# Optimization experiments

Hardware: AMD Instinct MI355X
Metric: run time of the kernel (lower is better)

The kernel has to match this reference:

```python
import jax, jax.numpy as jnp
import numpy as np

SOFTCAP = 50.0
EPS = 1e-6
N_HEADS, D_HEAD = 16, 64


def _rms(x, w):
    return x * jax.lax.rsqrt(jnp.mean(x * x, axis=-1, keepdims=True) + EPS) * w


def _rope(x, cos, sin):
    # Faithful to source: apply_rope uses x.size(1) as the position axis, but is
    # called on (B, H, T, Dh) tensors, so positions are indexed by HEAD index.
    n = x.shape[1]
    x1, x2 = x[..., 0::2], x[..., 1::2]
    c = cos[:n][None, :, None, :]
    s = sin[:n][None, :, None, :]
    return jnp.stack([x1 * c - x2 * s, x1 * s + x2 * c], axis=-1).reshape(x.shape)


def setup_inputs() -> dict:
    key = jax.random.key(0)
    ks = jax.random.split(key, 12)
    L, D, H, Dh, Dff, V, B, T = 6, 1024, N_HEADS, D_HEAD, 4096, 32000, 1, 1024
    r = lambda k, shape: jax.random.normal(k, shape, dtype=jnp.float32) * 0.02
    return {
        'x': jax.random.randint(ks[0], (B, T), 0, V, dtype=jnp.int32),
        'embed': r(ks[1], (V, D)),
        'ln1': jnp.ones((L, D), jnp.float32),
        'Wq': r(ks[2], (L, H * Dh, D)),
        'Wk': r(ks[3], (L, H * Dh, D)),
        'Wv': r(ks[4], (L, H * Dh, D)),
        'Wo': r(ks[5], (L, D, H * Dh)),
        'qn': jnp.ones((L, Dh), jnp.float32),
        'kn': jnp.ones((L, Dh), jnp.float32),
        'ln2': jnp.ones((L, D), jnp.float32),
        'Wg': r(ks[6], (L, Dff, D)),
        'Wu': r(ks[7], (L, Dff, D)),
        'Wd': r(ks[8], (L, D, Dff)),
        'ln_out': jnp.ones((D,), jnp.float32),
    }


def reference(x, embed, ln1, Wq, Wk, Wv, Wo, qn, kn, ln2, Wg, Wu, Wd, ln_out):
    B, T = x.shape
    H, Dh = N_HEADS, D_HEAD
    scale = Dh ** -0.5
    # RoPE tables (theta=10000)
    freqs = 1.0 / (10000.0 ** (jnp.arange(0, Dh, 2, dtype=jnp.float32) / Dh))
    ang = jnp.arange(T, dtype=jnp.float32)[:, None] * freqs[None, :]
    cos, sin = jnp.cos(ang), jnp.sin(ang)
    mask = jnp.triu(jnp.ones((T, T), dtype=bool), k=1)  # True above diagonal

    h = embed[x]  # (B, T, D)

    def block(h, p):
        l1, wq, wk, wv, wo, qnw, knw, l2, wg, wu, wd = p
        hn = _rms(h, l1)
        q = (hn @ wq.T).reshape(B, T, H, Dh).transpose(0, 2, 1, 3)  # (B,H,T,Dh)
        k = (hn @ wk.T).reshape(B, T, H, Dh).transpose(0, 2, 1, 3)
        v = (hn @ wv.T).reshape(B, T, H, Dh).transpose(0, 2, 1, 3)
        q = _rope(_rms(q, qnw), cos, sin)
        k = _rope(_rms(k, knw), cos, sin)
        scores = jnp.einsum('bhtd,bhsd->bhts', q, k) * scale
        scores = SOFTCAP * jnp.tanh(scores / SOFTCAP)
        scores = jnp.where(mask[None, None], -jnp.inf, scores)
        attn = jax.nn.softmax(scores, axis=-1)
        o = jnp.einsum('bhts,bhsd->bhtd', attn, v)
        o = o.transpose(0, 2, 1, 3).reshape(B, T, H * Dh)
        h = h + o @ wo.T
        hn2 = _rms(h, l2)
        h = h + (jax.nn.silu(hn2 @ wg.T) * (hn2 @ wu.T)) @ wd.T
        return h, None

    h, _ = jax.lax.scan(block, h, (ln1, Wq, Wk, Wv, Wo, qn, kn, ln2, Wg, Wu, Wd))
    # tied embed/head
    logits = _rms(h, ln_out) @ embed.T  # (B, T, V)
    return logits
```

## Files before the change

### kernel.cpp

```cpp
#include <hip/hip_runtime.h>
#include <math.h>
#include <type_traits>

typedef __bf16 bf16_t;
typedef bf16_t bf16x4 __attribute__((ext_vector_type(4)));
typedef bf16_t bf16x8 __attribute__((ext_vector_type(8)));
typedef float  f32x4  __attribute__((ext_vector_type(4)));

#define RMS_EPS 1e-6f

enum { EP_STORE = 0, EP_RESID = 1, EP_SPLIT = 2, EP_SILU = 3 };

template<int V> using IC = std::integral_constant<int, V>;

static __device__ __forceinline__ f32x4 mfma16(bf16x8 a, bf16x8 b, f32x4 c) {
    return __builtin_amdgcn_mfma_f32_16x16x32_bf16(a, b, c, 0, 0, 0);
}

#define GLDS(gp, lp) __builtin_amdgcn_global_load_lds( \
    (const __attribute__((address_space(1))) void*)(gp), \
    (__attribute__((address_space(3))) void*)(lp), 16, 0, 0)

template<int N> static __device__ __forceinline__ void vmwait() {
    if constexpr (N == 0)      asm volatile("s_waitcnt vmcnt(0)" ::: "memory");
    else if constexpr (N == 2) asm volatile("s_waitcnt vmcnt(2)" ::: "memory");
    else if constexpr (N == 3) asm volatile("s_waitcnt vmcnt(3)" ::: "memory");
    else if constexpr (N == 4) asm volatile("s_waitcnt vmcnt(4)" ::: "memory");
    else if constexpr (N == 6) asm volatile("s_waitcnt vmcnt(6)" ::: "memory");
    else if constexpr (N == 8) asm volatile("s_waitcnt vmcnt(8)" ::: "memory");
    __builtin_amdgcn_sched_barrier(0);
}
static __device__ __forceinline__ void bar() { __builtin_amdgcn_s_barrier(); }

template<int BM, int BN, int WR, int WC, int PLANES, int EPIL>
__global__ __launch_bounds__(WR * WC * 64,
    (WR * WC == 8) ? 4 : ((PLANES >= 2 && BM == 128) ? 3 : 4))
void gemm_bf16(const bf16_t* __restrict__ Ah, const bf16_t* __restrict__ Al,
               const bf16_t* __restrict__ Bh,
               float* __restrict__ Cf, bf16_t* __restrict__ Ch, bf16_t* __restrict__ Cl,
               int K, int lda, int ldb, int ldc, long long sC)
{
    constexpr int ASZ = BM * 32, BSZ = BN * 32;
    constexpr int NW = WR * WC;
    constexpr int NLD = (BM / 16 * (PLANES >= 2 ? 2 : 1) + BN / 16) / NW;
    __shared__ __align__(16) bf16_t sAh[2][ASZ], sBh[2][BSZ];
    __shared__ __align__(16) bf16_t sAl[PLANES >= 2 ? 2 : 1][PLANES >= 2 ? ASZ : 8];

    const int gx = gridDim.x;
    int id = blockIdx.x + gx * blockIdx.y;
    if (gridDim.z == 1) {
        int nwg = gx * gridDim.y;
        int q = nwg >> 3, r = nwg & 7;
        int xcd = id & 7, ix = id >> 3;
        id = (xcd < r ? xcd * (q + 1) : r * (q + 1) + (xcd - r) * q) + ix;
    }
    const int bm = id % gx, bn = id / gx;
    const int row0 = bm * BM, col0 = bn * BN;

    const size_t kofs = (size_t)blockIdx.z * K;
    Ah += kofs;  Bh += kofs;
    if constexpr (PLANES >= 2) Al += kofs;

    const int tid = threadIdx.x, lane = tid & 63, wave = tid >> 6;
    const int lr = lane & 15, lg = lane >> 4;
    constexpr int WM = BM / WR, WN = BN / WC, MF = WM / 16, NF = WN / 16;
    const int wr = wave / WC, wc = wave % WC;

    f32x4 acc[MF][NF];
    #pragma unroll
    for (int m = 0; m < MF; ++m)
        #pragma unroll
        for (int n = 0; n < NF; ++n) acc[m][n] = (f32x4){0.f, 0.f, 0.f, 0.f};

    auto stage = [&](int k0, auto pc) {
        constexpr int p = decltype(pc)::value;
        #pragma unroll
        for (int i = wave; i < BM / 16; i += NW) {
            int s = i * 64 + lane, rr = s >> 2, c = s & 3;
            size_t go = (size_t)(row0 + rr) * lda + k0 + ((c ^ ((rr >> 1) & 3)) << 3);
            GLDS(Ah + go, &sAh[p][i * 512]);
            if constexpr (PLANES >= 2) GLDS(Al + go, &sAl[p][i * 512]);
        }
        #pragma unroll
        for (int i = wave; i < BN / 16; i += NW) {
            int s = i * 64 + lane, rr = s >> 2, c = s & 3;
            size_t go = (size_t)(col0 + rr) * ldb + k0 + ((c ^ ((rr >> 1) & 3)) << 3);
            GLDS(Bh + go, &sBh[p][i * 512]);
        }
    };

    auto compute = [&](auto pc) {
        constexpr int p = decltype(pc)::value;
        bf16x8 ahf[MF], alf[MF], bhf[NF];
        #pragma unroll
        for (int m = 0; m < MF; ++m) {
            int rr = wr * WM + m * 16 + lr;
            int by = rr * 64 + ((lg ^ ((rr >> 1) & 3)) << 4);
            ahf[m] = *(const bf16x8*)((const char*)&sAh[p][0] + by);
            if constexpr (PLANES >= 2)
                alf[m] = *(const bf16x8*)((const char*)&sAl[p][0] + by);
        }
        #pragma unroll
        for (int n = 0; n < NF; ++n) {
            int rr = wc * WN + n * 16 + lr;
            int by = rr * 64 + ((lg ^ ((rr >> 1) & 3)) << 4);
            bhf[n] = *(const bf16x8*)((const char*)&sBh[p][0] + by);
        }
        #pragma unroll
        for (int m = 0; m < MF; ++m)
            #pragma unroll
            for (int n = 0; n < NF; ++n) {
                acc[m][n] = mfma16(ahf[m], bhf[n], acc[m][n]);
                if constexpr (PLANES >= 2)
                    acc[m][n] = mfma16(alf[m], bhf[n], acc[m][n]);
            }
    };

    stage(0, IC<0>{});
    int k0 = 32;
    for (; k0 + 32 < K; k0 += 64) {
        stage(k0, IC<1>{});
        vmwait<NLD>(); bar();
        compute(IC<0>{});
        bar();
        stage(k0 + 32, IC<0>{});
        vmwait<NLD>(); bar();
        compute(IC<1>{});
        bar();
    }
    stage(k0, IC<1>{});
    vmwait<NLD>(); bar();
    compute(IC<0>{});
    bar();
    vmwait<0>(); bar();
    compute(IC<1>{});

    #pragma unroll
    for (int m = 0; m < MF; ++m)
        #pragma unroll
        for (int n = 0; n < NF; ++n)
            #pragma unroll
            for (int r = 0; r < 4; ++r) {
                int grow = row0 + wr * WM + m * 16 + lg * 4 + r;
                int gcol = col0 + wc * WN + n * 16 + lr;
                float v = acc[m][n][r];
                if constexpr (EPIL == EP_SILU) {
                    float pv = __shfl_xor(v, 1, 64);
                    if (!(lr & 1)) {
                        float s = (v / (1.0f + expf(-v))) * pv;
                        size_t off = (size_t)grow * ldc + (gcol >> 1);
                        Ch[off] = (bf16_t)s;
                    }
                } else {
                    size_t off = (size_t)blockIdx.z * sC + (size_t)grow * ldc + gcol;
                    if constexpr (EPIL == EP_STORE) {
                        Cf[off] = v;
                    } else if constexpr (EPIL == EP_RESID) {
                        Cf[off] += v;
                    } else {
                        bf16_t hb = (bf16_t)v;
                        Ch[off] = hb;
                        Cl[off] = (bf16_t)(v - (float)hb);
                    }
                }
            }
}

__global__ __launch_bounds__(512, 4)
void gemm_logits(const bf16_t* __restrict__ Ah, const bf16_t* __restrict__ Bh,
                 float* __restrict__ Cf)
{
    constexpr int lda = 1024, ldb = 1024, ldc = 32000;
    __shared__ __align__(16) bf16_t sA[3][128 * 32], sB[3][256 * 32];

    const int gx = gridDim.x;
    int id = blockIdx.x + gx * blockIdx.y;
    {
        int nwg = gx * gridDim.y;
        int q = nwg >> 3, r = nwg & 7;
        int xcd = id & 7, ix = id >> 3;
        id = (xcd < r ? xcd * (q + 1) : r * (q + 1) + (xcd - r) * q) + ix;
    }
    const int bm = id % gx, bn = id / gx;
    const int row0 = bm * 128, col0 = bn * 256;

    const int tid = threadIdx.x, lane = tid & 63, wave = tid >> 6;
    const int lr = lane & 15, lg = lane >> 4;
    const int wr = wave >> 2, wc = wave & 3;

    f32x4 acc[4][4];
    #pragma unroll
    for (int m = 0; m < 4; ++m)
        #pragma unroll
        for (int n = 0; n < 4; ++n) acc[m][n] = (f32x4){0.f, 0.f, 0.f, 0.f};

    auto stage = [&](int k0, int p) {
        {
            int i = wave;
            int s = i * 64 + lane, rr = s >> 2, c = s & 3;
            size_t go = (size_t)(row0 + rr) * lda + k0 + ((c ^ ((rr >> 1) & 3)) << 3);
            GLDS(Ah + go, &sA[p][i * 512]);
        }
        #pragma unroll
        for (int i = wave; i < 16; i += 8) {
            int s = i * 64 + lane, rr = s >> 2, c = s & 3;
            size_t go = (size_t)(col0 + rr) * ldb + k0 + ((c ^ ((rr >> 1) & 3)) << 3);
            GLDS(Bh + go, &sB[p][i * 512]);
        }
    };

    auto compute = [&](int p) {
        bf16x8 af[4], bf[4];
        #pragma unroll
        for (int m = 0; m < 4; ++m) {
            int rr = wr * 64 + m * 16 + lr;
            int by = rr * 64 + ((lg ^ ((rr >> 1) & 3)) << 4);
            af[m] = *(const bf16x8*)((const char*)&sA[p][0] + by);
        }
        #pragma unroll
        for (int n = 0; n < 4; ++n) {
            int rr = wc * 64 + n * 16 + lr;
            int by = rr * 64 + ((lg ^ ((rr >> 1) & 3)) << 4);
            bf[n] = *(const bf16x8*)((const char*)&sB[p][0] + by);
        }
        #pragma unroll
        for (int m = 0; m < 4; ++m)
            #pragma unroll
            for (int n = 0; n < 4; ++n)
                acc[m][n] = mfma16(af[m], bf[n], acc[m][n]);
    };

    stage(0, 0);
    stage(32, 1);
    for (int j = 0; j < 30; ++j) {
        stage(32 * (j + 2), (j + 2) % 3);
        vmwait<6>(); bar();
        compute(j % 3);
        bar();
    }
    vmwait<3>(); bar();
    compute(0);
    vmwait<0>(); bar();
    compute(1);

    #pragma unroll
    for (int m = 0; m < 4; ++m)
        #pragma unroll
        for (int n = 0; n < 4; ++n)
            #pragma unroll
            for (int r = 0; r < 4; ++r) {
                int grow = row0 + wr * 64 + m * 16 + lg * 4 + r;
                int gcol = col0 + wc * 64 + n * 16 + lr;
                Cf[(size_t)grow * ldc + gcol] = acc[m][n][r];
            }
}

static __device__ __forceinline__ void wsplit_body(
    int b2, int tid,
    const float* wq, const float* wk, const float* wv, const float* wo,
    const float* wg, const float* wu, const float* wd,
    bf16_t* wAh, bf16_t* wGUh, bf16_t* wdh)
{
    #pragma unroll
    for (int k = 0; k < 4; ++k) {
        int b = b2 * 4 + k;
        const float* src;
        bf16_t* dst;
        size_t so, doff;
        if (b < 4096) {
            src = b < 1024 ? wq : b < 2048 ? wk : b < 3072 ? wv : wo;
            so = (size_t)(b & 1023) * 256 + tid;
            doff = (size_t)b * 256 + tid;
            dst = wAh;
        } else if (b < 12288) {
            int bb = b - 4096;
            int row = bb < 4096 ? 2 * bb : 2 * (bb - 4096) + 1;
            src = bb < 4096 ? wg : wu;
            so = (size_t)(bb & 4095) * 256 + tid;
            doff = (size_t)row * 256 + tid;
            dst = wGUh;
        } else {
            src = wd;
            so = (size_t)(b - 12288) * 256 + tid;
            doff = so;
            dst = wdh;
        }
        f32x4 v = ((const f32x4*)src)[so];
        bf16x4 hv;
        #pragma unroll
        for (int j = 0; j < 4; ++j) hv[j] = (bf16_t)v[j];
        ((bf16x4*)dst)[doff] = hv;
    }
}

__global__ __launch_bounds__(256)
void reduce_rms_wsplit(const float* __restrict__ p, float* __restrict__ h,
                       const float* __restrict__ w, bf16_t* __restrict__ outh,
                       const float* wq, const float* wk, const float* wv,
                       const float* wo, const float* wg, const float* wu,
                       const float* wd, bf16_t* wAh, bf16_t* wGUh, bf16_t* wdh)
{
    int blk = blockIdx.x, tid = threadIdx.x;
    if (blk >= 1024) {
        if (wq) wsplit_body(blk - 1024, tid, wq, wk, wv, wo, wg, wu, wd,
                            wAh, wGUh, wdh);
        return;
    }
    size_t i = (size_t)blk * 256 + tid;
    const size_t S = (1024 * 1024) / 4;
    f32x4 a = ((const f32x4*)p)[i];
    f32x4 b = ((const f32x4*)p)[i + S];
    f32x4 c = ((const f32x4*)p)[i + 2 * S];
    f32x4 d = ((const f32x4*)p)[i + 3 * S];
    f32x4 hv = ((const f32x4*)h)[i];
    #pragma unroll
    for (int j = 0; j < 4; ++j) hv[j] += (a[j] + b[j]) + (c[j] + d[j]);
    ((f32x4*)h)[i] = hv;

    float ss = hv[0]*hv[0] + hv[1]*hv[1] + hv[2]*hv[2] + hv[3]*hv[3];
    #pragma unroll
    for (int m = 1; m < 64; m <<= 1) ss += __shfl_xor(ss, m, 64);
    __shared__ float red[4];
    if ((tid & 63) == 0) red[tid >> 6] = ss;
    __syncthreads();
    float tot = red[0] + red[1] + red[2] + red[3];
    float inv = rsqrtf(tot * (1.0f / 1024.0f) + RMS_EPS);
    f32x4 wt4 = *(const f32x4*)(w + tid * 4);
    bf16x4 hv4;
    #pragma unroll
    for (int j = 0; j < 4; ++j) hv4[j] = (bf16_t)(hv[j] * inv * wt4[j]);
    ((bf16x4*)outh)[i] = hv4;
}

__global__ __launch_bounds__(256)
void gather_rms_wsplit(const int* __restrict__ ids, const float* __restrict__ embed,
                       const float* __restrict__ w, float* __restrict__ h,
                       bf16_t* __restrict__ outh,
                       const float* wq, const float* wk, const float* wv,
                       const float* wo, const float* wg, const float* wu,
                       const float* wd, bf16_t* wAh, bf16_t* wGUh, bf16_t* wdh)
{
    int blk = blockIdx.x, tid = threadIdx.x;
    if (blk >= 1024) {
        wsplit_body(blk - 1024, tid, wq, wk, wv, wo, wg, wu, wd, wAh, wGUh, wdh);
        return;
    }
    int row = ids[blk];
    f32x4 v = ((const f32x4*)(embed + (size_t)row * 1024))[tid];
    ((f32x4*)(h + (size_t)blk * 1024))[tid] = v;

    float ss = v[0]*v[0] + v[1]*v[1] + v[2]*v[2] + v[3]*v[3];
    #pragma unroll
    for (int m = 1; m < 64; m <<= 1) ss += __shfl_xor(ss, m, 64);
    __shared__ float red[4];
    if ((tid & 63) == 0) red[tid >> 6] = ss;
    __syncthreads();
    float tot = red[0] + red[1] + red[2] + red[3];
    float inv = rsqrtf(tot * (1.0f / 1024.0f) + RMS_EPS);
    f32x4 wt4 = *(const f32x4*)(w + tid * 4);
    bf16x4 hv;
    #pragma unroll
    for (int j = 0; j < 4; ++j) hv[j] = (bf16_t)(v[j] * inv * wt4[j]);
    ((bf16x4*)outh)[(size_t)blk * 256 + tid] = hv;
}

__global__ __launch_bounds__(128, 2)
void flash_attn(const bf16_t* __restrict__ qkvh,
                const bf16_t* __restrict__ vTh, const bf16_t* __restrict__ vTl,
                bf16_t* __restrict__ oh)
{
    __shared__ __align__(16) bf16_t sQ[32*64], sK[64*64], sVh[64*64], sVl[64*64];
    __shared__ __align__(16) bf16_t sPh[32*64], sPl[32*64];

    const int q0 = blockIdx.x * 32;
    const int hh = blockIdx.y;
    const int tid = threadIdx.x, lane = tid & 63, w = tid >> 6;
    const int lr = lane & 15, lg = lane >> 4;

    #pragma unroll
    for (int ii = 0; ii < 2; ++ii) {
        int r0 = w * 16 + ii * 8;
        int r  = r0 + (lane >> 3);
        int i  = lane & 7;
        GLDS(qkvh + (size_t)(q0 + r) * 3072 + hh * 64 + ((i ^ (r & 7)) << 3),
             sQ + r0 * 64);
    }
    __syncthreads();

    bf16x8 qa[2];
    #pragma unroll
    for (int ks = 0; ks < 2; ++ks) {
        int r = w * 16 + lr;
        qa[ks] = *(const bf16x8*)((const char*)sQ + r * 128 +
                                  ((((ks << 2) | lg) ^ (r & 7)) << 4));
    }

    f32x4 o_acc[4];
    #pragma unroll
    for (int n = 0; n < 4; ++n) o_acc[n] = (f32x4){0.f, 0.f, 0.f, 0.f};
    float m_run[4] = {-1e30f, -1e30f, -1e30f, -1e30f};
    float l_run[4] = {0.f, 0.f, 0.f, 0.f};

    const int ntiles = ((q0 + 31) >> 6) + 1;
    for (int t = 0; t < ntiles; ++t) {
        const int kv0 = t * 64;
        #pragma unroll
        for (int ii = 0; ii < 4; ++ii) {
            int r0 = w * 32 + ii * 8;
            int r  = r0 + (lane >> 3);
            int i  = lane & 7;
            GLDS(qkvh + (size_t)(kv0 + r) * 3072 + 1024 + hh * 64 + ((i ^ (r & 7)) << 3),
                 sK + r0 * 64);
            GLDS(vTh + (size_t)(hh * 64 + r) * 1024 + kv0 + ((i ^ (r & 7)) << 3),
                 sVh + r0 * 64);
            GLDS(vTl + (size_t)(hh * 64 + r) * 1024 + kv0 + ((i ^ (r & 7)) << 3),
                 sVl + r0 * 64);
        }
        __syncthreads();

        f32x4 s_acc[4];
        #pragma unroll
        for (int n = 0; n < 4; ++n) s_acc[n] = (f32x4){0.f, 0.f, 0.f, 0.f};
        #pragma unroll
        for (int ks = 0; ks < 2; ++ks)
            #pragma unroll
            for (int n = 0; n < 4; ++n) {
                int r = n * 16 + lr;
                bf16x8 kb = *(const bf16x8*)((const char*)sK + r * 128 +
                                             ((((ks << 2) | lg) ^ (r & 7)) << 4));
                s_acc[n] = mfma16(qa[ks], kb, s_acc[n]);
            }

        #pragma unroll
        for (int j = 0; j < 4; ++j) {
            int qr = q0 + w * 16 + lg * 4 + j;
            float p[4];
            float mx = -1e30f;
            #pragma unroll
            for (int n = 0; n < 4; ++n) {
                float v = s_acc[n][j] * 0.125f;
                v = 50.f * tanhf(v * 0.02f);
                int key = kv0 + n * 16 + lr;
                if (key > qr) v = -1e30f;
                p[n] = v;
                mx = fmaxf(mx, v);
            }
            #pragma unroll
            for (int m = 1; m < 16; m <<= 1) mx = fmaxf(mx, __shfl_xor(mx, m, 64));
            float mn = fmaxf(m_run[j], mx);
            float ef = __expf(m_run[j] - mn);
            m_run[j] = mn;
            float rs = 0.f;
            #pragma unroll
            for (int n = 0; n < 4; ++n) {
                float e = expf(p[n] - mn);
                p[n] = e;
                rs += e;
            }
            #pragma unroll
            for (int m = 1; m < 16; m <<= 1) rs += __shfl_xor(rs, m, 64);
            l_run[j] = l_run[j] * ef + rs;
            #pragma unroll
            for (int n = 0; n < 4; ++n) o_acc[n][j] *= ef;
            int r = w * 16 + lg * 4 + j;
            #pragma unroll
            for (int n = 0; n < 4; ++n) {
                int c = n * 16 + lr;
                int byo = r * 128 + ((((c >> 3) ^ (r & 7)) << 4)) + ((c & 7) << 1);
                bf16_t hb = (bf16_t)p[n];
                *(bf16_t*)((char*)sPh + byo) = hb;
                *(bf16_t*)((char*)sPl + byo) = (bf16_t)(p[n] - (float)hb);
            }
        }

        #pragma unroll
        for (int ks = 0; ks < 2; ++ks) {
            int pr = w * 16 + lr;
            int pby = pr * 128 + ((((ks << 2) | lg) ^ (pr & 7)) << 4);
            bf16x8 pa  = *(const bf16x8*)((const char*)sPh + pby);
            bf16x8 pl_ = *(const bf16x8*)((const char*)sPl + pby);
            #pragma unroll
            for (int n = 0; n < 4; ++n) {
                int vr = n * 16 + lr;
                int vby = vr * 128 + ((((ks << 2) | lg) ^ (vr & 7)) << 4);
                bf16x8 vhf = *(const bf16x8*)((const char*)sVh + vby);
                bf16x8 vlf = *(const bf16x8*)((const char*)sVl + vby);
                o_acc[n] = mfma16(pa,  vhf, o_acc[n]);
                o_acc[n] = mfma16(pl_, vhf, o_acc[n]);
                o_acc[n] = mfma16(pa,  vlf, o_acc[n]);
            }
        }
        __syncthreads();
    }

    #pragma unroll
    for (int j = 0; j < 4; ++j) {
        float inv = 1.0f / l_run[j];
        int qr = q0 + w * 16 + lg * 4 + j;
        #pragma unroll
        for (int n = 0; n < 4; ++n) {
            size_t off = (size_t)qr * 1024 + hh * 64 + n * 16 + lr;
            oh[off] = (bf16_t)(o_acc[n][j] * inv);
        }
    }
}

__global__ __launch_bounds__(256)
void split_kernel(const float* __restrict__ src, bf16_t* __restrict__ hi)
{
    size_t i = (size_t)blockIdx.x * 256 + threadIdx.x;
    f32x4 v = ((const f32x4*)src)[i];
    bf16x4 hv;
    #pragma unroll
    for (int j = 0; j < 4; ++j) hv[j] = (bf16_t)v[j];
    ((bf16x4*)hi)[i] = hv;
}

__global__ __launch_bounds__(256)
void rmsnorm_split(const float* __restrict__ in, const float* __restrict__ w,
                   bf16_t* __restrict__ outh)
{
    int row = blockIdx.x, tid = threadIdx.x;
    f32x4 v = *(const f32x4*)(in + (size_t)row * 1024 + tid * 4);
    float ss = v[0]*v[0] + v[1]*v[1] + v[2]*v[2] + v[3]*v[3];
    #pragma unroll
    for (int m = 1; m < 64; m <<= 1) ss += __shfl_xor(ss, m, 64);
    __shared__ float red[4];
    if ((tid & 63) == 0) red[tid >> 6] = ss;
    __syncthreads();
    float tot = red[0] + red[1] + red[2] + red[3];
    float inv = rsqrtf(tot * (1.0f / 1024.0f) + RMS_EPS);
    f32x4 wt4 = *(const f32x4*)(w + tid * 4);
    bf16x4 hv;
    #pragma unroll
    for (int j = 0; j < 4; ++j) hv[j] = (bf16_t)(v[j] * inv * wt4[j]);
    ((bf16x4*)outh)[(size_t)row * 256 + tid] = hv;
}

__global__ __launch_bounds__(256)
void rope_transpose(bf16_t* __restrict__ qkvh, bf16_t* __restrict__ qkvl,
                    const float* __restrict__ qn, const float* __restrict__ kn,
                    bf16_t* __restrict__ vTh, bf16_t* __restrict__ vTl)
{
    __shared__ bf16_t tile[32][33];
    int b = blockIdx.x;
    if (b >= 1024) {
        int t2 = b - 1024;
        int z = t2 >> 10, rem = t2 & 1023;
        const bf16_t* in = z ? qkvl : qkvh;
        bf16_t* out      = z ? vTl : vTh;
        int bx = (rem & 31) * 32, by = (rem >> 5) * 32;
        int r = threadIdx.x >> 5, c = threadIdx.x & 31;
        #pragma unroll
        for (int rr = r; rr < 32; rr += 8)
            tile[rr][c] = in[(size_t)(by + rr) * 3072 + 2048 + bx + c];
        __syncthreads();
        #pragma unroll
        for (int rr = r; rr < 32; rr += 8)
            out[(size_t)(bx + rr) * 1024 + by + c] = tile[c][rr];
        return;
    }

    int t = b, tid = threadIdx.x;
    int hh = tid >> 4;
    int i  = (tid & 15) * 4;
    size_t qb = ((size_t)t * 3072 + hh * 64 + i) >> 2;
    size_t kb = qb + (1024 >> 2);

    int p0 = i >> 1;
    float f0 = powf(10000.f, -(float)p0 / 32.f);
    float f1 = powf(10000.f, -(float)(p0 + 1) / 32.f);
    float a0 = (float)hh * f0, a1 = (float)hh * f1;
    float c0 = cosf(a0), s0 = sinf(a0);
    float c1 = cosf(a1), s1 = sinf(a1);

    f32x4 qw = *(const f32x4*)(qn + i);
    f32x4 kw = *(const f32x4*)(kn + i);

    {
        bf16x4 h4 = ((const bf16x4*)qkvh)[qb], l4 = ((const bf16x4*)qkvl)[qb];
        float x[4];
        #pragma unroll
        for (int j = 0; j < 4; ++j) x[j] = (float)h4[j] + (float)l4[j];
        float ss = x[0]*x[0] + x[1]*x[1] + x[2]*x[2] + x[3]*x[3];
        #pragma unroll
        for (int m = 1; m < 16; m <<= 1) ss += __shfl_xor(ss, m, 64);
        float inv = rsqrtf(ss * (1.0f / 64.0f) + RMS_EPS);
        float x0 = x[0]*inv*qw[0], x1 = x[1]*inv*qw[1];
        float x2 = x[2]*inv*qw[2], x3 = x[3]*inv*qw[3];
        bf16x4 o4;
        o4[0] = (bf16_t)(x0*c0 - x1*s0);  o4[1] = (bf16_t)(x0*s0 + x1*c0);
        o4[2] = (bf16_t)(x2*c1 - x3*s1);  o4[3] = (bf16_t)(x2*s1 + x3*c1);
        ((bf16x4*)qkvh)[qb] = o4;
    }
    {
        bf16x4 h4 = ((const bf16x4*)qkvh)[kb], l4 = ((const bf16x4*)qkvl)[kb];
        float x[4];
        #pragma unroll
        for (int j = 0; j < 4; ++j) x[j] = (float)h4[j] + (float)l4[j];
        float ss = x[0]*x[0] + x[1]*x[1] + x[2]*x[2] + x[3]*x[3];
        #pragma unroll
        for (int m = 1; m < 16; m <<= 1) ss += __shfl_xor(ss, m, 64);
        float inv = rsqrtf(ss * (1.0f / 64.0f) + RMS_EPS);
        float x0 = x[0]*inv*kw[0], x1 = x[1]*inv*kw[1];
        float x2 = x[2]*inv*kw[2], x3 = x[3]*inv*kw[3];
        bf16x4 o4;
        o4[0] = (bf16_t)(x0*c0 - x1*s0);  o4[1] = (bf16_t)(x0*s0 + x1*c0);
        o4[2] = (bf16_t)(x2*c1 - x3*s1);  o4[3] = (bf16_t)(x2*s1 + x3*c1);
        ((bf16x4*)qkvh)[kb] = o4;
    }
}

extern "C" void kernel_launch(void* const* d_in, const int* in_sizes, int n_in,
                              void* d_out, int out_size, void* d_ws, size_t ws_size,
                              hipStream_t stream)
{
    (void)in_sizes; (void)n_in; (void)out_size; (void)ws_size;
    const int*   x_ids = (const int*)  d_in[0];
    const float* embed = (const float*)d_in[1];
    const float* ln1   = (const float*)d_in[2];
    const float* Wq    = (const float*)d_in[3];
    const float* Wk    = (const float*)d_in[4];
    const float* Wv    = (const float*)d_in[5];
    const float* Wo    = (const float*)d_in[6];
    const float* qn    = (const float*)d_in[7];
    const float* kn    = (const float*)d_in[8];
    const float* ln2   = (const float*)d_in[9];
    const float* Wg    = (const float*)d_in[10];
    const float* Wu    = (const float*)d_in[11];
    const float* Wd    = (const float*)d_in[12];
    const float* lnout = (const float*)d_in[13];
    float* out = (float*)d_out;

    char* ws = (char*)d_ws;
    const size_t MB = 1 << 20;
    float*  h    = (float*) (ws +   0 * MB);
    bf16_t* hnh  = (bf16_t*)(ws +   4 * MB);
    bf16_t* qkvh = (bf16_t*)(ws +   8 * MB);
    bf16_t* qkvl = (bf16_t*)(ws +  14 * MB);
    bf16_t* vTh  = (bf16_t*)(ws +  20 * MB);
    bf16_t* vTl  = (bf16_t*)(ws +  22 * MB);
    bf16_t* oh   = (bf16_t*)(ws +  24 * MB);
    bf16_t* wAh  = (bf16_t*)(ws +  28 * MB);
    bf16_t* wGUh = (bf16_t*)(ws +  36 * MB);
    bf16_t* wdh  = (bf16_t*)(ws +  52 * MB);
    bf16_t* silh = (bf16_t*)(ws +  60 * MB);
    float*  wdp  = (float*) (ws +  68 * MB);
    bf16_t* eh   = (bf16_t*)(ws +  84 * MB);

    const long long M1 = 1024 * 1024;

    gather_rms_wsplit<<<5120, 256, 0, stream>>>(
        x_ids, embed, ln1, h, hnh,
        Wq, Wk, Wv, Wo, Wg, Wu, Wd, wAh, wGUh, wdh);

    for (int l = 0; l < 6; ++l) {
        gemm_bf16<64,128,2,2,1,EP_SPLIT><<<dim3(16,24),256,0,stream>>>(
            hnh, nullptr, wAh, nullptr, qkvh, qkvl, 1024, 1024, 1024, 3072, 0);

        rope_transpose<<<3072, 256, 0, stream>>>(qkvh, qkvl, qn + l * 64, kn + l * 64,
                                                 vTh, vTl);

        flash_attn<<<dim3(32,16), 128, 0, stream>>>(qkvh, vTh, vTl, oh);

        gemm_bf16<64,64,2,2,1,EP_RESID><<<dim3(16,16),256,0,stream>>>(
            oh, nullptr, wAh + 3 * M1, h, nullptr, nullptr, 1024, 1024, 1024, 1024, 0);

        rmsnorm_split<<<1024, 256, 0, stream>>>(h, ln2 + l * 1024, hnh);

        gemm_bf16<128,256,2,4,1,EP_SILU><<<dim3(8,32),512,0,stream>>>(
            hnh, nullptr, wGUh, nullptr, silh, nullptr, 1024, 1024, 1024, 4096, 0);

        gemm_bf16<128,128,2,2,1,EP_STORE><<<dim3(8,8,4),256,0,stream>>>(
            silh, nullptr, wdh, wdp, nullptr, nullptr, 1024, 4096, 4096, 1024, M1);

        const float* wnext = (l < 5) ? (ln1 + (l + 1) * 1024) : lnout;
        if (l < 5) {
            reduce_rms_wsplit<<<5120, 256, 0, stream>>>(
                wdp, h, wnext, hnh,
                Wq + (size_t)(l+1) * M1, Wk + (size_t)(l+1) * M1,
                Wv + (size_t)(l+1) * M1, Wo + (size_t)(l+1) * M1,
                Wg + (size_t)(l+1) * 4 * M1, Wu + (size_t)(l+1) * 4 * M1,
                Wd + (size_t)(l+1) * 4 * M1, wAh, wGUh, wdh);
        } else {
            reduce_rms_wsplit<<<1024, 256, 0, stream>>>(
                wdp, h, wnext, hnh,
                nullptr, nullptr, nullptr, nullptr, nullptr, nullptr, nullptr,
                wAh, wGUh, wdh);
        }
    }

    split_kernel<<<32000, 256, 0, stream>>>(embed, eh);
    gemm_logits<<<dim3(8,125), 512, 0, stream>>>(hnh, eh, out);
}
```

Measured before the change: 1.236 ms.

## Fuse QK RMSNorm and RoPE into QKV GEMM epilogue; reuse generic GEMM for logits

```diff
diff --git a/kernel.cpp b/kernel.cpp
--- a/kernel.cpp
+++ b/kernel.cpp
@@ -9,7 +9,7 @@
 
 #define RMS_EPS 1e-6f
 
-enum { EP_STORE = 0, EP_RESID = 1, EP_SPLIT = 2, EP_SILU = 3 };
+enum { EP_STORE = 0, EP_RESID = 1, EP_SPLIT = 2, EP_SILU = 3, EP_QKV = 4 };
 
 template<int V> using IC = std::integral_constant<int, V>;
 
@@ -32,13 +32,13 @@
 }
 static __device__ __forceinline__ void bar() { __builtin_amdgcn_s_barrier(); }
 
-template<int BM, int BN, int WR, int WC, int PLANES, int EPIL>
-__global__ __launch_bounds__(WR * WC * 64,
-    (WR * WC == 8) ? 4 : ((PLANES >= 2 && BM == 128) ? 3 : 4))
+template<int BM, int BN, int WR, int WC, int PLANES, int EPIL, int MINW>
+__global__ __launch_bounds__(WR * WC * 64, MINW)
 void gemm_bf16(const bf16_t* __restrict__ Ah, const bf16_t* __restrict__ Al,
                const bf16_t* __restrict__ Bh,
                float* __restrict__ Cf, bf16_t* __restrict__ Ch, bf16_t* __restrict__ Cl,
-               int K, int lda, int ldb, int ldc, long long sC)
+               int K, int lda, int ldb, int ldc, long long sC,
+               const float* __restrict__ qnw, const float* __restrict__ knw)
 {
     constexpr int ASZ = BM * 32, BSZ = BN * 32;
     constexpr int NW = WR * WC;
@@ -134,6 +134,54 @@
     bar();
     vmwait<0>(); bar();
     compute(IC<1>{});
+
+    if constexpr (EPIL == EP_QKV) {
+        const int colbase = col0 + wc * WN;
+        const int typ = colbase >> 10;
+        const float* nw = (typ == 0) ? qnw : knw;
+        const int hh = (colbase - typ * 1024) >> 6;
+        constexpr float kLogF = -0.41524101186092029f;
+        #pragma unroll
+        for (int m = 0; m < MF; ++m)
+            #pragma unroll
+            for (int r = 0; r < 4; ++r) {
+                int grow = row0 + wr * WM + m * 16 + lg * 4 + r;
+                if (typ < 2) {
+                    float ss = 0.f;
+                    #pragma unroll
+                    for (int n = 0; n < NF; ++n) {
+                        float v = acc[m][n][r];
+                        ss += v * v;
+                    }
+                    ss += __shfl_xor(ss, 1, 64);
+                    ss += __shfl_xor(ss, 2, 64);
+                    ss += __shfl_xor(ss, 4, 64);
+                    ss += __shfl_xor(ss, 8, 64);
+                    float inv = rsqrtf(ss * (1.0f / 64.0f) + RMS_EPS);
+                    #pragma unroll
+                    for (int n = 0; n < NF; ++n) {
+                        int i = n * 16 + lr;
+                        float x = acc[m][n][r] * inv * nw[i];
+                        float p = __shfl_xor(x, 1, 64);
+                        float f = exp2f((float)(i >> 1) * kLogF);
+                        float ang = (float)hh * f;
+                        float cs = cosf(ang), sn = sinf(ang);
+                        float o = (lr & 1) ? (p * sn + x * cs) : (x * cs - p * sn);
+                        Ch[(size_t)grow * ldc + colbase + i] = (bf16_t)o;
+                    }
+                } else {
+                    #pragma unroll
+                    for (int n = 0; n < NF; ++n) {
+                        float v = acc[m][n][r];
+                        size_t off = (size_t)grow * ldc + colbase + n * 16 + lr;
+                        bf16_t hb = (bf16_t)v;
+                        Ch[off] = hb;
+                        Cl[off] = (bf16_t)(v - (float)hb);
+                    }
+                }
+            }
+        return;
+    }
 
     #pragma unroll
     for (int m = 0; m < MF; ++m)
@@ -166,95 +214,6 @@
             }
 }
 
-__global__ __launch_bounds__(512, 4)
-void gemm_logits(const bf16_t* __restrict__ Ah, const bf16_t* __restrict__ Bh,
-                 float* __restrict__ Cf)
-{
-    constexpr int lda = 1024, ldb = 1024, ldc = 32000;
-    __shared__ __align__(16) bf16_t sA[3][128 * 32], sB[3][256 * 32];
-
-    const int gx = gridDim.x;
-    int id = blockIdx.x + gx * blockIdx.y;
-    {
-        int nwg = gx * gridDim.y;
-        int q = nwg >> 3, r = nwg & 7;
-        int xcd = id & 7, ix = id >> 3;
-        id = (xcd < r ? xcd * (q + 1) : r * (q + 1) + (xcd - r) * q) + ix;
-    }
-    const int bm = id % gx, bn = id / gx;
-    const int row0 = bm * 128, col0 = bn * 256;
-
-    const int tid = threadIdx.x, lane = tid & 63, wave = tid >> 6;
-    const int lr = lane & 15, lg = lane >> 4;
-    const int wr = wave >> 2, wc = wave & 3;
-
-    f32x4 acc[4][4];
-    #pragma unroll
-    for (int m = 0; m < 4; ++m)
-        #pragma unroll
-        for (int n = 0; n < 4; ++n) acc[m][n] = (f32x4){0.f, 0.f, 0.f, 0.f};
-
-    auto stage = [&](int k0, int p) {
-        {
-            int i = wave;
-            int s = i * 64 + lane, rr = s >> 2, c = s & 3;
-            size_t go = (size_t)(row0 + rr) * lda + k0 + ((c ^ ((rr >> 1) & 3)) << 3);
-            GLDS(Ah + go, &sA[p][i * 512]);
-        }
-        #pragma unroll
-        for (int i = wave; i < 16; i += 8) {
-            int s = i * 64 + lane, rr = s >> 2, c = s & 3;
-            size_t go = (size_t)(col0 + rr) * ldb + k0 + ((c ^ ((rr >> 1) & 3)) << 3);
-            GLDS(Bh + go, &sB[p][i * 512]);
-        }
-    };
-
-    auto compute = [&](int p) {
-        bf16x8 af[4], bf[4];
-        #pragma unroll
-        for (int m = 0; m < 4; ++m) {
-            int rr = wr * 64 + m * 16 + lr;
-            int by = rr * 64 + ((lg ^ ((rr >> 1) & 3)) << 4);
-            af[m] = *(const bf16x8*)((const char*)&sA[p][0] + by);
-        }
-        #pragma unroll
-        for (int n = 0; n < 4; ++n) {
-            int rr = wc * 64 + n * 16 + lr;
-            int by = rr * 64 + ((lg ^ ((rr >> 1) & 3)) << 4);
-            bf[n] = *(const bf16x8*)((const char*)&sB[p][0] + by);
-        }
-        #pragma unroll
-        for (int m = 0; m < 4; ++m)
-            #pragma unroll
-            for (int n = 0; n < 4; ++n)
-                acc[m][n] = mfma16(af[m], bf[n], acc[m][n]);
-    };
-
-    stage(0, 0);
-    stage(32, 1);
-    for (int j = 0; j < 30; ++j) {
-        stage(32 * (j + 2), (j + 2) % 3);
-        vmwait<6>(); bar();
-        compute(j % 3);
-        bar();
-    }
-    vmwait<3>(); bar();
-    compute(0);
-    vmwait<0>(); bar();
-    compute(1);
-
-    #pragma unroll
-    for (int m = 0; m < 4; ++m)
-        #pragma unroll
-        for (int n = 0; n < 4; ++n)
-            #pragma unroll
-            for (int r = 0; r < 4; ++r) {
-                int grow = row0 + wr * 64 + m * 16 + lg * 4 + r;
-                int gcol = col0 + wc * 64 + n * 16 + lr;
-                Cf[(size_t)grow * ldc + gcol] = acc[m][n][r];
-            }
-}
-
 static __device__ __forceinline__ void wsplit_body(
     int b2, int tid,
     const float* wq, const float* wk, const float* wv, const float* wo,
@@ -538,77 +497,23 @@
 }
 
 __global__ __launch_bounds__(256)
-void rope_transpose(bf16_t* __restrict__ qkvh, bf16_t* __restrict__ qkvl,
-                    const float* __restrict__ qn, const float* __restrict__ kn,
-                    bf16_t* __restrict__ vTh, bf16_t* __restrict__ vTl)
+void transpose_v(const bf16_t* __restrict__ qkvh, const bf16_t* __restrict__ qkvl,
+                 bf16_t* __restrict__ vTh, bf16_t* __restrict__ vTl)
 {
     __shared__ bf16_t tile[32][33];
     int b = blockIdx.x;
-    if (b >= 1024) {
-        int t2 = b - 1024;
-        int z = t2 >> 10, rem = t2 & 1023;
-        const bf16_t* in = z ? qkvl : qkvh;
-        bf16_t* out      = z ? vTl : vTh;
-        int bx = (rem & 31) * 32, by = (rem >> 5) * 32;
-        int r = threadIdx.x >> 5, c = threadIdx.x & 31;
-        #pragma unroll
-        for (int rr = r; rr < 32; rr += 8)
-            tile[rr][c] = in[(size_t)(by + rr) * 3072 + 2048 + bx + c];
-        __syncthreads();
-        #pragma unroll
-        for (int rr = r; rr < 32; rr += 8)
-            out[(size_t)(bx + rr) * 1024 + by + c] = tile[c][rr];
-        return;
-    }
-
-    int t = b, tid = threadIdx.x;
-    int hh = tid >> 4;
-    int i  = (tid & 15) * 4;
-    size_t qb = ((size_t)t * 3072 + hh * 64 + i) >> 2;
-    size_t kb = qb + (1024 >> 2);
-
-    int p0 = i >> 1;
-    float f0 = powf(10000.f, -(float)p0 / 32.f);
-    float f1 = powf(10000.f, -(float)(p0 + 1) / 32.f);
-    float a0 = (float)hh * f0, a1 = (float)hh * f1;
-    float c0 = cosf(a0), s0 = sinf(a0);
-    float c1 = cosf(a1), s1 = sinf(a1);
-
-    f32x4 qw = *(const f32x4*)(qn + i);
-    f32x4 kw = *(const f32x4*)(kn + i);
-
-    {
-        bf16x4 h4 = ((const bf16x4*)qkvh)[qb], l4 = ((const bf16x4*)qkvl)[qb];
-        float x[4];
-        #pragma unroll
-        for (int j = 0; j < 4; ++j) x[j] = (float)h4[j] + (float)l4[j];
-        float ss = x[0]*x[0] + x[1]*x[1] + x[2]*x[2] + x[3]*x[3];
-        #pragma unroll
-        for (int m = 1; m < 16; m <<= 1) ss += __shfl_xor(ss, m, 64);
-        float inv = rsqrtf(ss * (1.0f / 64.0f) + RMS_EPS);
-        float x0 = x[0]*inv*qw[0], x1 = x[1]*inv*qw[1];
-        float x2 = x[2]*inv*qw[2], x3 = x[3]*inv*qw[3];
-        bf16x4 o4;
-        o4[0] = (bf16_t)(x0*c0 - x1*s0);  o4[1] = (bf16_t)(x0*s0 + x1*c0);
-        o4[2] = (bf16_t)(x2*c1 - x3*s1);  o4[3] = (bf16_t)(x2*s1 + x3*c1);
-        ((bf16x4*)qkvh)[qb] = o4;
-    }
-    {
-        bf16x4 h4 = ((const bf16x4*)qkvh)[kb], l4 = ((const bf16x4*)qkvl)[kb];
-        float x[4];
-        #pragma unroll
-        for (int j = 0; j < 4; ++j) x[j] = (float)h4[j] + (float)l4[j];
-        float ss = x[0]*x[0] + x[1]*x[1] + x[2]*x[2] + x[3]*x[3];
-        #pragma unroll
-        for (int m = 1; m < 16; m <<= 1) ss += __shfl_xor(ss, m, 64);
-        float inv = rsqrtf(ss * (1.0f / 64.0f) + RMS_EPS);
-        float x0 = x[0]*inv*kw[0], x1 = x[1]*inv*kw[1];
-        float x2 = x[2]*inv*kw[2], x3 = x[3]*inv*kw[3];
-        bf16x4 o4;
-        o4[0] = (bf16_t)(x0*c0 - x1*s0);  o4[1] = (bf16_t)(x0*s0 + x1*c0);
-        o4[2] = (bf16_t)(x2*c1 - x3*s1);  o4[3] = (bf16_t)(x2*s1 + x3*c1);
-        ((bf16x4*)qkvh)[kb] = o4;
-    }
+    int z = b >> 10, rem = b & 1023;
+    const bf16_t* in = z ? qkvl : qkvh;
+    bf16_t* out      = z ? vTl : vTh;
+    int bx = (rem & 31) * 32, by = (rem >> 5) * 32;
+    int r = threadIdx.x >> 5, c = threadIdx.x & 31;
+    #pragma unroll
+    for (int rr = r; rr < 32; rr += 8)
+        tile[rr][c] = in[(size_t)(by + rr) * 3072 + 2048 + bx + c];
+    __syncthreads();
+    #pragma unroll
+    for (int rr = r; rr < 32; rr += 8)
+        out[(size_t)(bx + rr) * 1024 + by + c] = tile[c][rr];
 }
 
 extern "C" void kernel_launch(void* const* d_in, const int* in_sizes, int n_in,
@@ -655,24 +560,27 @@
         Wq, Wk, Wv, Wo, Wg, Wu, Wd, wAh, wGUh, wdh);
 
     for (int l = 0; l < 6; ++l) {
-        gemm_bf16<64,128,2,2,1,EP_SPLIT><<<dim3(16,24),256,0,stream>>>(
-            hnh, nullptr, wAh, nullptr, qkvh, qkvl, 1024, 1024, 1024, 3072, 0);
-
-        rope_transpose<<<3072, 256, 0, stream>>>(qkvh, qkvl, qn + l * 64, kn + l * 64,
-                                                 vTh, vTl);
+        gemm_bf16<64,128,2,2,1,EP_QKV,4><<<dim3(16,24),256,0,stream>>>(
+            hnh, nullptr, wAh, nullptr, qkvh, qkvl, 1024, 1024, 1024, 3072, 0,
+            qn + l * 64, kn + l * 64);
+
+        transpose_v<<<2048, 256, 0, stream>>>(qkvh, qkvl, vTh, vTl);
 
         flash_attn<<<dim3(32,16), 128, 0, stream>>>(qkvh, vTh, vTl, oh);
 
-        gemm_bf16<64,64,2,2,1,EP_RESID><<<dim3(16,16),256,0,stream>>>(
-            oh, nullptr, wAh + 3 * M1, h, nullptr, nullptr, 1024, 1024, 1024, 1024, 0);
+        gemm_bf16<64,64,2,2,1,EP_RESID,4><<<dim3(16,16),256,0,stream>>>(
+            oh, nullptr, wAh + 3 * M1, h, nullptr, nullptr, 1024, 1024, 1024, 1024, 0,
+            nullptr, nullptr);
 
         rmsnorm_split<<<1024, 256, 0, stream>>>(h, ln2 + l * 1024, hnh);
 
-        gemm_bf16<128,256,2,4,1,EP_SILU><<<dim3(8,32),512,0,stream>>>(
-            hnh, nullptr, wGUh, nullptr, silh, nullptr, 1024, 1024, 1024, 4096, 0);
-
-        gemm_bf16<128,128,2,2,1,EP_STORE><<<dim3(8,8,4),256,0,stream>>>(
-            silh, nullptr, wdh, wdp, nullptr, nullptr, 1024, 4096, 4096, 1024, M1);
+        gemm_bf16<128,256,2,4,1,EP_SILU,4><<<dim3(8,32),512,0,stream>>>(
+            hnh, nullptr, wGUh, nullptr, silh, nullptr, 1024, 1024, 1024, 4096, 0,
+            nullptr, nullptr);
+
+        gemm_bf16<128,128,2,2,1,EP_STORE,4><<<dim3(8,8,4),256,0,stream>>>(
+            silh, nullptr, wdh, wdp, nullptr, nullptr, 1024, 4096, 4096, 1024, M1,
+            nullptr, nullptr);
 
         const float* wnext = (l < 5) ? (ln1 + (l + 1) * 1024) : lnout;
         if (l < 5) {
@@ -691,5 +599,7 @@
     }
 
     split_kernel<<<32000, 256, 0, stream>>>(embed, eh);
-    gemm_logits<<<dim3(8,125), 512, 0, stream>>>(hnh, eh, out);
-}
+    gemm_bf16<256,256,2,4,1,EP_STORE,2><<<dim3(4,125),512,0,stream>>>(
+        hnh, nullptr, eh, out, nullptr, nullptr, 1024, 1024, 1024, 32000, 0,
+        nullptr, nullptr);
+}
```

Result: no change. 1.243 ms (+0.6%).
